# Optimization experiments

Hardware: AMD Instinct MI355X
Metric: run time of the kernel (lower is better)

## Reference

```python
import jax, jax.numpy as jnp
import numpy as np

B, N, F, E = 2048, 64, 32, 5
U1, U2, UA = 128, 64, 128

def setup_inputs() -> dict:
    key = jax.random.key(0)
    ks = jax.random.split(key, 16)
    inp = {
        'adjacency': jax.random.uniform(ks[0], (B, N, N, E), dtype=jnp.float32),
        'hidden': jnp.zeros((B, 1), dtype=jnp.float32),
        'node': jax.random.normal(ks[1], (B, N, F), dtype=jnp.float32),
        # conv layer 1: per-edge-type dense F->U1 (stacked), plus node dense F->U1
        'W1': jax.random.normal(ks[2], (E - 1, F, U1), dtype=jnp.float32) * 0.05,
        'b1': jnp.zeros((E - 1, U1), dtype=jnp.float32),
        'V1': jax.random.normal(ks[3], (F, U1), dtype=jnp.float32) * 0.05,
        'c1': jnp.zeros((U1,), dtype=jnp.float32),
        # conv layer 2: annotations (U1+F)->U2, node F->U2
        'W2': jax.random.normal(ks[4], (E - 1, U1 + F, U2), dtype=jnp.float32) * 0.05,
        'b2': jnp.zeros((E - 1, U2), dtype=jnp.float32),
        'V2': jax.random.normal(ks[5], (F, U2), dtype=jnp.float32) * 0.05,
        'c2': jnp.zeros((U2,), dtype=jnp.float32),
        # aggregation: (U2+F)->UA gates
        'Wi': jax.random.normal(ks[6], (U2 + F, UA), dtype=jnp.float32) * 0.05,
        'bi': jnp.zeros((UA,), dtype=jnp.float32),
        'Wj': jax.random.normal(ks[7], (U2 + F, UA), dtype=jnp.float32) * 0.05,
        'bj': jnp.zeros((UA,), dtype=jnp.float32),
    }
    return inp


def _gconv(adj_t, annotations, node, W, b, V, c):
    # adj_t: [B,E-1,N,N]; annotations: [B,N,Fa]; node: [B,N,F]
    h = jnp.einsum('bnf,efu->benu', annotations, W) + b[None, :, None, :]
    h = jnp.einsum('bemn,benu->bemu', adj_t, h)          # adjacency-weighted sum
    out = h.sum(axis=1) + node @ V + c                   # [B,N,U]
    return jnp.tanh(out)


def reference(adjacency, hidden, node, W1, b1, V1, c1, W2, b2, V2, c2, Wi, bi, Wj, bj):
    # drop edge type 0, transpose to [B,E-1,N,N]
    adj_t = jnp.transpose(adjacency[:, :, :, 1:], (0, 3, 1, 2))
    # hidden is rank-2 at entry -> first layer uses node only
    h1 = _gconv(adj_t, node, node, W1, b1, V1, c1)                       # [B,N,U1]
    h2 = _gconv(adj_t, jnp.concatenate((h1, node), -1), node, W2, b2, V2, c2)  # [B,N,U2]
    # encoder-level annotations: (output, node) since hidden is rank-2
    ann = jnp.concatenate((h2, node), -1)                                # [B,N,U2+F]
    i = jax.nn.sigmoid(ann @ Wi + bi)
    j = jnp.tanh(ann @ Wj + bj)
    out = jnp.tanh(jnp.sum(i * j, axis=1))                               # [B,UA]
    return out
```

## Files before the change

kernel.cpp:

```cpp
#include <hip/hip_runtime.h>

typedef _Float16 f16;
typedef f16  f16x8 __attribute__((ext_vector_type(8)));
typedef f16  f16x4 __attribute__((ext_vector_type(4)));
typedef float f32x4 __attribute__((ext_vector_type(4)));
typedef unsigned int u32;

#define W1T_HI 0
#define W1T_LO 16384
#define V1T_HI 32768
#define V1T_LO 36864
#define W2T_HI 40960
#define W2T_LO 81920
#define V2T_HI 122880
#define V2T_LO 124928
#define WIT_HI 126976
#define WIT_LO 139264
#define WJT_HI 151552
#define WJT_LO 163840
#define WS_SRC 88064

#define ADJB_HI 0
#define ADJB_LO 32768
#define ANNB_HI 49152
#define ANNB_LO 65536
#define PTB     73728
#define LDS_BYTES 81920

__device__ __forceinline__ f32x4 mfma16(f16x8 a, f16x8 b, f32x4 c){
  return __builtin_amdgcn_mfma_f32_16x16x32_f16(a, b, c, 0, 0, 0);
}
__device__ __forceinline__ float fast_tanh(float x){
  float e = __expf(2.f * x);
  return 1.f - 2.f * __builtin_amdgcn_rcpf(e + 1.f);
}
__device__ __forceinline__ float fast_sigmoid(float x){
  return __builtin_amdgcn_rcpf(1.f + __expf(-x));
}

__device__ __forceinline__ unsigned char enc1(float lo){
  f16 h = (f16)lo;
  unsigned short u = __builtin_bit_cast(unsigned short, h);
  return (unsigned char)(((u32)u + 0x80u) >> 8);
}
__device__ __forceinline__ void enc8(unsigned char* p, const float* lo){
  u32 a = 0, b = 0;
  #pragma unroll
  for (int j = 0; j < 4; ++j) a |= (u32)enc1(lo[j]) << (8*j);
  #pragma unroll
  for (int j = 0; j < 4; ++j) b |= (u32)enc1(lo[4+j]) << (8*j);
  uint2 v = {a, b};
  *(uint2*)p = v;
}
__device__ __forceinline__ u32 enc4(const float* lo){
  return (u32)enc1(lo[0]) | ((u32)enc1(lo[1]) << 8)
       | ((u32)enc1(lo[2]) << 16) | ((u32)enc1(lo[3]) << 24);
}
__device__ __forceinline__ f16x8 dec8(const unsigned char* p){
  uint2 d = *(const uint2*)p;
  u32 w[4];
  w[0] = __builtin_amdgcn_perm(0u, d.x, 0x010c000cu);
  w[1] = __builtin_amdgcn_perm(0u, d.x, 0x030c020cu);
  w[2] = __builtin_amdgcn_perm(0u, d.y, 0x010c000cu);
  w[3] = __builtin_amdgcn_perm(0u, d.y, 0x030c020cu);
  f16x8 r; __builtin_memcpy(&r, w, 16);
  return r;
}

__global__ void prep_weights(const float* __restrict__ W1, const float* __restrict__ V1,
                             const float* __restrict__ W2, const float* __restrict__ V2,
                             const float* __restrict__ Wi, const float* __restrict__ Wj,
                             f16* __restrict__ ws){
  int i = blockIdx.x * 256 + threadIdx.x;
  if (i >= WS_SRC) return;
  float v; int hi_off, lo_off, idx;
  int j = i;
  if (j < 16384){ int e = j >> 12, u = (j >> 5) & 127, f = j & 31;
    v = W1[(e*32 + f)*128 + u]; hi_off = W1T_HI; lo_off = W1T_LO; idx = j; }
  else if ((j -= 16384) < 4096){ int u = j >> 5, f = j & 31;
    v = V1[f*128 + u]; hi_off = V1T_HI; lo_off = V1T_LO; idx = j; }
  else if ((j -= 4096) < 40960){ int e = j / 10240, r = j % 10240, u = r / 160, k = r % 160;
    v = W2[e*10240 + k*64 + u]; hi_off = W2T_HI; lo_off = W2T_LO; idx = j; }
  else if ((j -= 40960) < 2048){ int u = j >> 5, f = j & 31;
    v = V2[f*64 + u]; hi_off = V2T_HI; lo_off = V2T_LO; idx = j; }
  else if ((j -= 2048) < 12288){ int ua = j / 96, k = j % 96;
    v = Wi[k*128 + ua]; hi_off = WIT_HI; lo_off = WIT_LO; idx = j; }
  else { j -= 12288; int ua = j / 96, k = j % 96;
    v = Wj[k*128 + ua]; hi_off = WJT_HI; lo_off = WJT_LO; idx = j; }
  f16 h = (f16)v;
  ws[hi_off + idx] = h;
  ws[lo_off + idx] = (f16)(v - (float)h);
}

__global__ __launch_bounds__(256, 2) void encoder_main(
    const float* __restrict__ adj, const float* __restrict__ node,
    const float* __restrict__ b1, const float* __restrict__ c1,
    const float* __restrict__ b2, const float* __restrict__ c2,
    const float* __restrict__ bi, const float* __restrict__ bj,
    const f16* __restrict__ wb, float* __restrict__ out)
{
  extern __shared__ unsigned char ldsb[];
  f16* adjh            = (f16*)(ldsb + ADJB_HI);
  unsigned char* adjl  = ldsb + ADJB_LO;
  f16* annh            = (f16*)(ldsb + ANNB_HI);
  unsigned char* annl  = ldsb + ANNB_LO;
  unsigned char* ptb   = ldsb + PTB;
  f16* nodeH           = (f16*)(ldsb + PTB);
  f16* nodeLo          = (f16*)(ldsb + PTB + 4096);

  const int tid  = threadIdx.x;
  const int w    = tid >> 6;
  const int lane = tid & 63;
  const int q    = lane >> 4;
  const int l15  = lane & 15;
  const int b    = blockIdx.x;
  const f32x4 z4 = {0.f, 0.f, 0.f, 0.f};

  {
    const float* ap = adj + (size_t)b * 20480;
    #pragma unroll
    for (int i = 0; i < 8; ++i){
      int fu = tid + 256*i;
      int e = fu >> 9, m = (fu >> 3) & 63, uc = fu & 7;
      const float* p = ap + (m*64 + uc*8)*5 + e + 1;
      float v[8], lo[8]; f16x8 hi;
      #pragma unroll
      for (int jj = 0; jj < 8; ++jj) v[jj] = p[jj*5];
      #pragma unroll
      for (int jj = 0; jj < 8; ++jj){
        f16 h = (f16)v[jj]; hi[jj] = h; lo[jj] = v[jj] - (float)h;
      }
      int off = e*4096 + m*64 + ((uc ^ (m & 7)) * 8);
      *(f16x8*)&adjh[off] = hi;
      enc8(&adjl[off], lo);
    }
    const float* np = node + (size_t)b * 2048 + (tid & 63)*32 + (tid >> 6)*8;
    float4 a = *(const float4*)np, c = *(const float4*)(np + 4);
    float v[8] = {a.x, a.y, a.z, a.w, c.x, c.y, c.z, c.w};
    f16x8 hi, lo;
    #pragma unroll
    for (int jj = 0; jj < 8; ++jj){
      f16 h = (f16)v[jj]; hi[jj] = h; lo[jj] = (f16)(v[jj] - (float)h);
    }
    int n = tid & 63, un = tid >> 6;
    *(f16x8*)&nodeH [n*32 + ((un ^ (n & 3)) * 8)] = hi;
    *(f16x8*)&nodeLo[n*32 + ((un ^ (n & 3)) * 8)] = lo;
  }
  __syncthreads();

  f16x8 anh[4], anl[4];
  #pragma unroll
  for (int mt = 0; mt < 4; ++mt){
    anh[mt] = *(const f16x8*)&nodeH [(mt*16 + l15)*32 + ((q ^ (l15 & 3)) * 8)];
    anl[mt] = *(const f16x8*)&nodeLo[(mt*16 + l15)*32 + ((q ^ (l15 & 3)) * 8)];
  }
  __syncthreads();

  const int ptrow  = (w*16 + l15) * 128;
  const int ptlrow = (w*16 + l15) * 128;

  f32x4 acc1[4][2];
  #pragma unroll
  for (int mt = 0; mt < 4; ++mt){ acc1[mt][0] = z4; acc1[mt][1] = z4; }

  #pragma unroll
  for (int e = 0; e < 4; ++e){
    f16x8 ah[2][4], al[2][4];
    #pragma unroll
    for (int ks = 0; ks < 2; ++ks)
      #pragma unroll
      for (int mt = 0; mt < 4; ++mt){
        int off = e*4096 + (mt*16 + l15)*64 + (((ks*4 + q) ^ (l15 & 7)) * 8);
        ah[ks][mt] = *(const f16x8*)&adjh[off];
        al[ks][mt] = dec8(&adjl[off]);
      }
    #pragma unroll
    for (int ut = 0; ut < 2; ++ut){
      const int u = w*32 + ut*16 + l15;
      f16x8 wh = *(const f16x8*)&wb[W1T_HI + (e*128 + u)*32 + q*8];
      f16x8 wl = *(const f16x8*)&wb[W1T_LO + (e*128 + u)*32 + q*8];
      float bias = b1[e*128 + u];
      #pragma unroll
      for (int mt = 0; mt < 4; ++mt){
        f32x4 pf = mfma16(anh[mt], wh, z4);
        pf = mfma16(anl[mt], wh, pf);
        pf = mfma16(anh[mt], wl, pf);
        f16x4 ph; float lo4[4];
        #pragma unroll
        for (int r = 0; r < 4; ++r){
          float v = pf[r] + bias;
          f16 h = (f16)v; ph[r] = h; lo4[r] = v - (float)h;
        }
        int unit = ((mt*2 + (q >> 1)) ^ (l15 & 7));
        *(f16x4*)(ptb + ptrow + unit*16 + (q & 1)*8) = ph;
        *(u32*)(annl + ptlrow + unit*8 + (q & 1)*4) = enc4(lo4);
      }
      #pragma unroll
      for (int ks = 0; ks < 2; ++ks){
        int pu = ((ks*4 + q) ^ (l15 & 7));
        f16x8 bph = *(const f16x8*)(ptb + ptrow + pu*16);
        f16x8 bpl = dec8(annl + ptlrow + pu*8);
        #pragma unroll
        for (int mt = 0; mt < 4; ++mt){
          acc1[mt][ut] = mfma16(ah[ks][mt], bph, acc1[mt][ut]);
          acc1[mt][ut] = mfma16(al[ks][mt], bph, acc1[mt][ut]);
          acc1[mt][ut] = mfma16(ah[ks][mt], bpl, acc1[mt][ut]);
        }
      }
    }
  }
  __syncthreads();

  #pragma unroll
  for (int ut = 0; ut < 2; ++ut){
    const int u = w*32 + ut*16 + l15;
    f16x8 wh = *(const f16x8*)&wb[V1T_HI + u*32 + q*8];
    f16x8 wl = *(const f16x8*)&wb[V1T_LO + u*32 + q*8];
    float cv = c1[u];
    #pragma unroll
    for (int mt = 0; mt < 4; ++mt){
      f32x4 a = acc1[mt][ut];
      a = mfma16(anh[mt], wh, a);
      a = mfma16(anl[mt], wh, a);
      a = mfma16(anh[mt], wl, a);
      #pragma unroll
      for (int r = 0; r < 4; ++r){
        float h = fast_tanh(a[r] + cv);
        f16 hh = (f16)h;
        int row = mt*16 + q*4 + r;
        int unit = ((u >> 3) ^ (row & 7));
        annh[row*128 + unit*8 + (u & 7)] = hh;
        annl[row*128 + unit*8 + (u & 7)] = enc1(h - (float)hh);
      }
    }
  }
  __syncthreads();

  const int u2 = w*16 + l15;
  f32x4 qf[4][4];
  #pragma unroll
  for (int mt = 0; mt < 4; ++mt){
    f16x8 axh[4], axl[4];
    #pragma unroll
    for (int ks = 0; ks < 4; ++ks){
      int off = (mt*16 + l15)*128 + (((ks*4 + q) ^ (l15 & 7)) * 8);
      axh[ks] = *(const f16x8*)&annh[off];
      axl[ks] = dec8(&annl[off]);
    }
    #pragma unroll
    for (int e = 0; e < 4; ++e){
      const f16* w2h = &wb[W2T_HI + (e*64 + u2)*160];
      const f16* w2l = &wb[W2T_LO + (e*64 + u2)*160];
      f16x8 wnh = *(const f16x8*)&w2h[4*32 + q*8];
      f16x8 wnl = *(const f16x8*)&w2l[4*32 + q*8];
      f32x4 t = mfma16(anh[mt], wnh, z4);
      t = mfma16(anl[mt], wnh, t);
      t = mfma16(anh[mt], wnl, t);
      #pragma unroll
      for (int ks = 0; ks < 4; ++ks){
        f16x8 wh = *(const f16x8*)&w2h[ks*32 + q*8];
        f16x8 wl = *(const f16x8*)&w2l[ks*32 + q*8];
        t = mfma16(axh[ks], wh, t);
        t = mfma16(axl[ks], wh, t);
        t = mfma16(axh[ks], wl, t);
      }
      qf[e][mt] = t;
    }
  }
  __syncthreads();

  f32x4 acc2[4];
  #pragma unroll
  for (int mt = 0; mt < 4; ++mt) acc2[mt] = z4;
  #pragma unroll
  for (int e = 0; e < 4; ++e){
    float bias = b2[e*64 + u2];
    #pragma unroll
    for (int mt = 0; mt < 4; ++mt){
      f16x4 ph; float lo4[4];
      #pragma unroll
      for (int r = 0; r < 4; ++r){
        float v = qf[e][mt][r] + bias;
        f16 h = (f16)v; ph[r] = h; lo4[r] = v - (float)h;
      }
      int unit = ((mt*2 + (q >> 1)) ^ (l15 & 7));
      *(f16x4*)(ptb + ptrow + unit*16 + (q & 1)*8) = ph;
      *(u32*)(annl + ptlrow + unit*8 + (q & 1)*4) = enc4(lo4);
    }
    #pragma unroll
    for (int ks = 0; ks < 2; ++ks){
      int pu = ((ks*4 + q) ^ (l15 & 7));
      f16x8 bph = *(const f16x8*)(ptb + ptrow + pu*16);
      f16x8 bpl = dec8(annl + ptlrow + pu*8);
      #pragma unroll
      for (int mt = 0; mt < 4; ++mt){
        int off = e*4096 + (mt*16 + l15)*64 + (((ks*4 + q) ^ (l15 & 7)) * 8);
        f16x8 ah = *(const f16x8*)&adjh[off];
        f16x8 al = dec8(&adjl[off]);
        acc2[mt] = mfma16(ah, bph, acc2[mt]);
        acc2[mt] = mfma16(al, bph, acc2[mt]);
        acc2[mt] = mfma16(ah, bpl, acc2[mt]);
      }
    }
  }
  {
    f16x8 wh = *(const f16x8*)&wb[V2T_HI + u2*32 + q*8];
    f16x8 wl = *(const f16x8*)&wb[V2T_LO + u2*32 + q*8];
    #pragma unroll
    for (int mt = 0; mt < 4; ++mt){
      acc2[mt] = mfma16(anh[mt], wh, acc2[mt]);
      acc2[mt] = mfma16(anl[mt], wh, acc2[mt]);
      acc2[mt] = mfma16(anh[mt], wl, acc2[mt]);
    }
  }
  {
    float cv = c2[u2];
    const int uc = 64 + u2;
    #pragma unroll
    for (int mt = 0; mt < 4; ++mt)
      #pragma unroll
      for (int r = 0; r < 4; ++r){
        float h = fast_tanh(acc2[mt][r] + cv);
        f16 hh = (f16)h;
        int row = mt*16 + q*4 + r;
        int unit = ((uc >> 3) ^ (row & 7));
        annh[row*128 + unit*8 + (uc & 7)] = hh;
        annl[row*128 + unit*8 + (uc & 7)] = enc1(h - (float)hh);
      }
  }
  __syncthreads();

  f16x8 wih[2][3], wil[2][3], wjh[2][3], wjl[2][3];
  float bib[2], bjb[2];
  #pragma unroll
  for (int ut = 0; ut < 2; ++ut){
    const int ua = w*32 + ut*16 + l15;
    #pragma unroll
    for (int ks = 0; ks < 3; ++ks){
      wih[ut][ks] = *(const f16x8*)&wb[WIT_HI + ua*96 + ks*32 + q*8];
      wil[ut][ks] = *(const f16x8*)&wb[WIT_LO + ua*96 + ks*32 + q*8];
      wjh[ut][ks] = *(const f16x8*)&wb[WJT_HI + ua*96 + ks*32 + q*8];
      wjl[ut][ks] = *(const f16x8*)&wb[WJT_LO + ua*96 + ks*32 + q*8];
    }
    bib[ut] = bi[ua]; bjb[ut] = bj[ua];
  }
  float s[2] = {0.f, 0.f};
  #pragma unroll
  for (int mt = 0; mt < 4; ++mt){
    f16x8 gh[2], gl[2];
    #pragma unroll
    for (int ks = 0; ks < 2; ++ks){
      int off = (mt*16 + l15)*128 + (((8 + ks*4 + q) ^ (l15 & 7)) * 8);
      gh[ks] = *(const f16x8*)&annh[off];
      gl[ks] = dec8(&annl[off]);
    }
    #pragma unroll
    for (int ut = 0; ut < 2; ++ut){
      f32x4 ia = mfma16(anh[mt], wih[ut][2], z4);
      ia = mfma16(anl[mt], wih[ut][2], ia);
      ia = mfma16(anh[mt], wil[ut][2], ia);
      f32x4 ja = mfma16(anh[mt], wjh[ut][2], z4);
      ja = mfma16(anl[mt], wjh[ut][2], ja);
      ja = mfma16(anh[mt], wjl[ut][2], ja);
      #pragma unroll
      for (int ks = 0; ks < 2; ++ks){
        ia = mfma16(gh[ks], wih[ut][ks], ia);
        ia = mfma16(gl[ks], wih[ut][ks], ia);
        ia = mfma16(gh[ks], wil[ut][ks], ia);
        ja = mfma16(gh[ks], wjh[ut][ks], ja);
        ja = mfma16(gl[ks], wjh[ut][ks], ja);
        ja = mfma16(gh[ks], wjl[ut][ks], ja);
      }
      #pragma unroll
      for (int r = 0; r < 4; ++r)
        s[ut] += fast_sigmoid(ia[r] + bib[ut]) * fast_tanh(ja[r] + bjb[ut]);
    }
  }
  #pragma unroll
  for (int ut = 0; ut < 2; ++ut){
    float t = s[ut];
    t += __shfl_xor(t, 16);
    t += __shfl_xor(t, 32);
    if (q == 0) out[(size_t)b*128 + (w*32 + ut*16 + l15)] = fast_tanh(t);
  }
}

extern "C" void kernel_launch(void* const* d_in, const int* in_sizes, int n_in,
                              void* d_out, int out_size, void* d_ws, size_t ws_size,
                              hipStream_t stream) {
  (void)in_sizes; (void)n_in; (void)out_size; (void)ws_size;
  const float* adj  = (const float*)d_in[0];
  const float* node = (const float*)d_in[2];
  const float* W1   = (const float*)d_in[3];
  const float* b1   = (const float*)d_in[4];
  const float* V1   = (const float*)d_in[5];
  const float* c1   = (const float*)d_in[6];
  const float* W2   = (const float*)d_in[7];
  const float* b2   = (const float*)d_in[8];
  const float* V2   = (const float*)d_in[9];
  const float* c2   = (const float*)d_in[10];
  const float* Wi   = (const float*)d_in[11];
  const float* bi   = (const float*)d_in[12];
  const float* Wj   = (const float*)d_in[13];
  const float* bj   = (const float*)d_in[14];
  f16* wb    = (f16*)d_ws;
  float* out = (float*)d_out;

  hipFuncSetAttribute((const void*)encoder_main,
                      hipFuncAttributeMaxDynamicSharedMemorySize, LDS_BYTES);

  prep_weights<<<(WS_SRC + 255) / 256, 256, 0, stream>>>(W1, V1, W2, V2, Wi, Wj, wb);
  encoder_main<<<2048, 256, LDS_BYTES, stream>>>(adj, node, b1, c1, b2, c2, bi, bj, wb, out);
}
```

Before: 366.2 us.

## Split edge types across two wave groups with 512-thread blocks and LDS reduction

Doubles the block to 8 waves and splits the four edge types so each group of four waves handles two, then reduces the partial accumulators of both graph-conv layers through an LDS scratch buffer. Per-wave scratch for the intermediate products is remapped into the node and annotation regions, and the aggregation stage gives each wave 16 output units. The aim is more parallelism per sample to hide latency. The cost is extra barriers and LDS traffic for the cross-group reduction, plus higher register pressure under the new launch bounds.

```diff
diff --git a/kernel.cpp b/kernel.cpp
--- a/kernel.cpp
+++ b/kernel.cpp
@@ -92,7 +92,7 @@
   ws[lo_off + idx] = (f16)(v - (float)h);
 }
 
-__global__ __launch_bounds__(256, 2) void encoder_main(
+__global__ __launch_bounds__(512, 4) void encoder_main(
     const float* __restrict__ adj, const float* __restrict__ node,
     const float* __restrict__ b1, const float* __restrict__ c1,
     const float* __restrict__ b2, const float* __restrict__ c2,
@@ -104,7 +104,7 @@
   unsigned char* adjl  = ldsb + ADJB_LO;
   f16* annh            = (f16*)(ldsb + ANNB_HI);
   unsigned char* annl  = ldsb + ANNB_LO;
-  unsigned char* ptb   = ldsb + PTB;
+  float* scr           = (float*)(ldsb + ANNB_HI);
   f16* nodeH           = (f16*)(ldsb + PTB);
   f16* nodeLo          = (f16*)(ldsb + PTB + 4096);
 
@@ -113,14 +113,21 @@
   const int lane = tid & 63;
   const int q    = lane >> 4;
   const int l15  = lane & 15;
+  const int eg   = w >> 2;
+  const int w4   = w & 3;
   const int b    = blockIdx.x;
   const f32x4 z4 = {0.f, 0.f, 0.f, 0.f};
 
+  unsigned char* ptb = ldsb + ((w < 4) ? (PTB + w*2048) : (ANNB_HI + (w - 4)*2048));
+  unsigned char* ptl = ldsb + ANNB_LO + w*1024;
+  const int ptrow  = l15 * 128;
+  const int ptlrow = l15 * 64;
+
   {
     const float* ap = adj + (size_t)b * 20480;
     #pragma unroll
-    for (int i = 0; i < 8; ++i){
-      int fu = tid + 256*i;
+    for (int i = 0; i < 4; ++i){
+      int fu = tid + 512*i;
       int e = fu >> 9, m = (fu >> 3) & 63, uc = fu & 7;
       const float* p = ap + (m*64 + uc*8)*5 + e + 1;
       float v[8], lo[8]; f16x8 hi;
@@ -134,17 +141,19 @@
       *(f16x8*)&adjh[off] = hi;
       enc8(&adjl[off], lo);
     }
-    const float* np = node + (size_t)b * 2048 + (tid & 63)*32 + (tid >> 6)*8;
-    float4 a = *(const float4*)np, c = *(const float4*)(np + 4);
-    float v[8] = {a.x, a.y, a.z, a.w, c.x, c.y, c.z, c.w};
-    f16x8 hi, lo;
-    #pragma unroll
-    for (int jj = 0; jj < 8; ++jj){
-      f16 h = (f16)v[jj]; hi[jj] = h; lo[jj] = (f16)(v[jj] - (float)h);
-    }
-    int n = tid & 63, un = tid >> 6;
-    *(f16x8*)&nodeH [n*32 + ((un ^ (n & 3)) * 8)] = hi;
-    *(f16x8*)&nodeLo[n*32 + ((un ^ (n & 3)) * 8)] = lo;
+    if (tid < 256){
+      const float* np = node + (size_t)b * 2048 + (tid & 63)*32 + (tid >> 6)*8;
+      float4 a = *(const float4*)np, c = *(const float4*)(np + 4);
+      float v[8] = {a.x, a.y, a.z, a.w, c.x, c.y, c.z, c.w};
+      f16x8 hi, lo;
+      #pragma unroll
+      for (int jj = 0; jj < 8; ++jj){
+        f16 h = (f16)v[jj]; hi[jj] = h; lo[jj] = (f16)(v[jj] - (float)h);
+      }
+      int n = tid & 63, un = tid >> 6;
+      *(f16x8*)&nodeH [n*32 + ((un ^ (n & 3)) * 8)] = hi;
+      *(f16x8*)&nodeLo[n*32 + ((un ^ (n & 3)) * 8)] = lo;
+    }
   }
   __syncthreads();
 
@@ -156,15 +165,13 @@
   }
   __syncthreads();
 
-  const int ptrow  = (w*16 + l15) * 128;
-  const int ptlrow = (w*16 + l15) * 128;
-
   f32x4 acc1[4][2];
   #pragma unroll
   for (int mt = 0; mt < 4; ++mt){ acc1[mt][0] = z4; acc1[mt][1] = z4; }
 
   #pragma unroll
-  for (int e = 0; e < 4; ++e){
+  for (int i = 0; i < 2; ++i){
+    const int e = eg*2 + i;
     f16x8 ah[2][4], al[2][4];
     #pragma unroll
     for (int ks = 0; ks < 2; ++ks)
@@ -176,7 +183,7 @@
       }
     #pragma unroll
     for (int ut = 0; ut < 2; ++ut){
-      const int u = w*32 + ut*16 + l15;
+      const int u = w4*32 + ut*16 + l15;
       f16x8 wh = *(const f16x8*)&wb[W1T_HI + (e*128 + u)*32 + q*8];
       f16x8 wl = *(const f16x8*)&wb[W1T_LO + (e*128 + u)*32 + q*8];
       float bias = b1[e*128 + u];
@@ -193,13 +200,13 @@
         }
         int unit = ((mt*2 + (q >> 1)) ^ (l15 & 7));
         *(f16x4*)(ptb + ptrow + unit*16 + (q & 1)*8) = ph;
-        *(u32*)(annl + ptlrow + unit*8 + (q & 1)*4) = enc4(lo4);
+        *(u32*)(ptl + ptlrow + unit*8 + (q & 1)*4) = enc4(lo4);
       }
       #pragma unroll
       for (int ks = 0; ks < 2; ++ks){
         int pu = ((ks*4 + q) ^ (l15 & 7));
         f16x8 bph = *(const f16x8*)(ptb + ptrow + pu*16);
-        f16x8 bpl = dec8(annl + ptlrow + pu*8);
+        f16x8 bpl = dec8(ptl + ptlrow + pu*8);
         #pragma unroll
         for (int mt = 0; mt < 4; ++mt){
           acc1[mt][ut] = mfma16(ah[ks][mt], bph, acc1[mt][ut]);
@@ -211,33 +218,67 @@
   }
   __syncthreads();
 
-  #pragma unroll
-  for (int ut = 0; ut < 2; ++ut){
-    const int u = w*32 + ut*16 + l15;
-    f16x8 wh = *(const f16x8*)&wb[V1T_HI + u*32 + q*8];
-    f16x8 wl = *(const f16x8*)&wb[V1T_LO + u*32 + q*8];
-    float cv = c1[u];
-    #pragma unroll
-    for (int mt = 0; mt < 4; ++mt){
-      f32x4 a = acc1[mt][ut];
-      a = mfma16(anh[mt], wh, a);
-      a = mfma16(anl[mt], wh, a);
-      a = mfma16(anh[mt], wl, a);
-      #pragma unroll
-      for (int r = 0; r < 4; ++r){
-        float h = fast_tanh(a[r] + cv);
-        f16 hh = (f16)h;
-        int row = mt*16 + q*4 + r;
-        int unit = ((u >> 3) ^ (row & 7));
-        annh[row*128 + unit*8 + (u & 7)] = hh;
-        annl[row*128 + unit*8 + (u & 7)] = enc1(h - (float)hh);
-      }
-    }
-  }
-  __syncthreads();
-
-  const int u2 = w*16 + l15;
-  f32x4 qf[4][4];
+  if (eg == 0){
+    #pragma unroll
+    for (int ut = 0; ut < 2; ++ut){
+      const int u = w4*32 + ut*16 + l15;
+      f16x8 wh = *(const f16x8*)&wb[V1T_HI + u*32 + q*8];
+      f16x8 wl = *(const f16x8*)&wb[V1T_LO + u*32 + q*8];
+      #pragma unroll
+      for (int mt = 0; mt < 4; ++mt){
+        acc1[mt][ut] = mfma16(anh[mt], wh, acc1[mt][ut]);
+        acc1[mt][ut] = mfma16(anl[mt], wh, acc1[mt][ut]);
+        acc1[mt][ut] = mfma16(anh[mt], wl, acc1[mt][ut]);
+      }
+    }
+  } else {
+    #pragma unroll
+    for (int mt = 0; mt < 4; ++mt)
+      #pragma unroll
+      for (int ut = 0; ut < 2; ++ut)
+        #pragma unroll
+        for (int r = 0; r < 4; ++r){
+          int n = mt*16 + q*4 + r;
+          int u = w4*32 + ut*16 + l15;
+          scr[n*128 + (u ^ ((n & 4) << 2))] = acc1[mt][ut][r];
+        }
+  }
+  __syncthreads();
+  if (eg == 0){
+    #pragma unroll
+    for (int mt = 0; mt < 4; ++mt)
+      #pragma unroll
+      for (int ut = 0; ut < 2; ++ut)
+        #pragma unroll
+        for (int r = 0; r < 4; ++r){
+          int n = mt*16 + q*4 + r;
+          int u = w4*32 + ut*16 + l15;
+          acc1[mt][ut][r] += scr[n*128 + (u ^ ((n & 4) << 2))];
+        }
+  }
+  __syncthreads();
+  if (eg == 0){
+    #pragma unroll
+    for (int ut = 0; ut < 2; ++ut){
+      const int u = w4*32 + ut*16 + l15;
+      float cv = c1[u];
+      #pragma unroll
+      for (int mt = 0; mt < 4; ++mt)
+        #pragma unroll
+        for (int r = 0; r < 4; ++r){
+          float h = fast_tanh(acc1[mt][ut][r] + cv);
+          f16 hh = (f16)h;
+          int row = mt*16 + q*4 + r;
+          int unit = ((u >> 3) ^ (row & 7));
+          annh[row*128 + unit*8 + (u & 7)] = hh;
+          annl[row*128 + unit*8 + (u & 7)] = enc1(h - (float)hh);
+        }
+    }
+  }
+  __syncthreads();
+
+  const int u2 = w4*16 + l15;
+  f32x4 qf[2][4];
   #pragma unroll
   for (int mt = 0; mt < 4; ++mt){
     f16x8 axh[4], axl[4];
@@ -248,7 +289,8 @@
       axl[ks] = dec8(&annl[off]);
     }
     #pragma unroll
-    for (int e = 0; e < 4; ++e){
+    for (int i = 0; i < 2; ++i){
+      const int e = eg*2 + i;
       const f16* w2h = &wb[W2T_HI + (e*64 + u2)*160];
       const f16* w2l = &wb[W2T_LO + (e*64 + u2)*160];
       f16x8 wnh = *(const f16x8*)&w2h[4*32 + q*8];
@@ -264,7 +306,7 @@
         t = mfma16(axl[ks], wh, t);
         t = mfma16(axh[ks], wl, t);
       }
-      qf[e][mt] = t;
+      qf[i][mt] = t;
     }
   }
   __syncthreads();
@@ -273,25 +315,26 @@
   #pragma unroll
   for (int mt = 0; mt < 4; ++mt) acc2[mt] = z4;
   #pragma unroll
-  for (int e = 0; e < 4; ++e){
+  for (int i = 0; i < 2; ++i){
+    const int e = eg*2 + i;
     float bias = b2[e*64 + u2];
     #pragma unroll
     for (int mt = 0; mt < 4; ++mt){
       f16x4 ph; float lo4[4];
       #pragma unroll
       for (int r = 0; r < 4; ++r){
-        float v = qf[e][mt][r] + bias;
+        float v = qf[i][mt][r] + bias;
         f16 h = (f16)v; ph[r] = h; lo4[r] = v - (float)h;
       }
       int unit = ((mt*2 + (q >> 1)) ^ (l15 & 7));
       *(f16x4*)(ptb + ptrow + unit*16 + (q & 1)*8) = ph;
-      *(u32*)(annl + ptlrow + unit*8 + (q & 1)*4) = enc4(lo4);
+      *(u32*)(ptl + ptlrow + unit*8 + (q & 1)*4) = enc4(lo4);
     }
     #pragma unroll
     for (int ks = 0; ks < 2; ++ks){
       int pu = ((ks*4 + q) ^ (l15 & 7));
       f16x8 bph = *(const f16x8*)(ptb + ptrow + pu*16);
-      f16x8 bpl = dec8(annl + ptlrow + pu*8);
+      f16x8 bpl = dec8(ptl + ptlrow + pu*8);
       #pragma unroll
       for (int mt = 0; mt < 4; ++mt){
         int off = e*4096 + (mt*16 + l15)*64 + (((ks*4 + q) ^ (l15 & 7)) * 8);
@@ -303,7 +346,8 @@
       }
     }
   }
-  {
+  __syncthreads();
+  if (eg == 0){
     f16x8 wh = *(const f16x8*)&wb[V2T_HI + u2*32 + q*8];
     f16x8 wl = *(const f16x8*)&wb[V2T_LO + u2*32 + q*8];
     #pragma unroll
@@ -312,8 +356,27 @@
       acc2[mt] = mfma16(anl[mt], wh, acc2[mt]);
       acc2[mt] = mfma16(anh[mt], wl, acc2[mt]);
     }
-  }
-  {
+  } else {
+    #pragma unroll
+    for (int mt = 0; mt < 4; ++mt)
+      #pragma unroll
+      for (int r = 0; r < 4; ++r){
+        int n = mt*16 + q*4 + r;
+        scr[n*64 + (u2 ^ ((n & 4) << 2))] = acc2[mt][r];
+      }
+  }
+  __syncthreads();
+  if (eg == 0){
+    #pragma unroll
+    for (int mt = 0; mt < 4; ++mt)
+      #pragma unroll
+      for (int r = 0; r < 4; ++r){
+        int n = mt*16 + q*4 + r;
+        acc2[mt][r] += scr[n*64 + (u2 ^ ((n & 4) << 2))];
+      }
+  }
+  __syncthreads();
+  if (eg == 0){
     float cv = c2[u2];
     const int uc = 64 + u2;
     #pragma unroll
@@ -330,21 +393,17 @@
   }
   __syncthreads();
 
-  f16x8 wih[2][3], wil[2][3], wjh[2][3], wjl[2][3];
-  float bib[2], bjb[2];
-  #pragma unroll
-  for (int ut = 0; ut < 2; ++ut){
-    const int ua = w*32 + ut*16 + l15;
-    #pragma unroll
-    for (int ks = 0; ks < 3; ++ks){
-      wih[ut][ks] = *(const f16x8*)&wb[WIT_HI + ua*96 + ks*32 + q*8];
-      wil[ut][ks] = *(const f16x8*)&wb[WIT_LO + ua*96 + ks*32 + q*8];
-      wjh[ut][ks] = *(const f16x8*)&wb[WJT_HI + ua*96 + ks*32 + q*8];
-      wjl[ut][ks] = *(const f16x8*)&wb[WJT_LO + ua*96 + ks*32 + q*8];
-    }
-    bib[ut] = bi[ua]; bjb[ut] = bj[ua];
-  }
-  float s[2] = {0.f, 0.f};
+  const int ua = w*16 + l15;
+  f16x8 wih[3], wil[3], wjh[3], wjl[3];
+  #pragma unroll
+  for (int ks = 0; ks < 3; ++ks){
+    wih[ks] = *(const f16x8*)&wb[WIT_HI + ua*96 + ks*32 + q*8];
+    wil[ks] = *(const f16x8*)&wb[WIT_LO + ua*96 + ks*32 + q*8];
+    wjh[ks] = *(const f16x8*)&wb[WJT_HI + ua*96 + ks*32 + q*8];
+    wjl[ks] = *(const f16x8*)&wb[WJT_LO + ua*96 + ks*32 + q*8];
+  }
+  float bib = bi[ua], bjb = bj[ua];
+  float s = 0.f;
   #pragma unroll
   for (int mt = 0; mt < 4; ++mt){
     f16x8 gh[2], gl[2];
@@ -354,35 +413,28 @@
       gh[ks] = *(const f16x8*)&annh[off];
       gl[ks] = dec8(&annl[off]);
     }
-    #pragma unroll
-    for (int ut = 0; ut < 2; ++ut){
-      f32x4 ia = mfma16(anh[mt], wih[ut][2], z4);
-      ia = mfma16(anl[mt], wih[ut][2], ia);
-      ia = mfma16(anh[mt], wil[ut][2], ia);
-      f32x4 ja = mfma16(anh[mt], wjh[ut][2], z4);
-      ja = mfma16(anl[mt], wjh[ut][2], ja);
-      ja = mfma16(anh[mt], wjl[ut][2], ja);
-      #pragma unroll
-      for (int ks = 0; ks < 2; ++ks){
-        ia = mfma16(gh[ks], wih[ut][ks], ia);
-        ia = mfma16(gl[ks], wih[ut][ks], ia);
-        ia = mfma16(gh[ks], wil[ut][ks], ia);
-        ja = mfma16(gh[ks], wjh[ut][ks], ja);
-        ja = mfma16(gl[ks], wjh[ut][ks], ja);
-        ja = mfma16(gh[ks], wjl[ut][ks], ja);
-      }
-      #pragma unroll
-      for (int r = 0; r < 4; ++r)
-        s[ut] += fast_sigmoid(ia[r] + bib[ut]) * fast_tanh(ja[r] + bjb[ut]);
-    }
-  }
-  #pragma unroll
-  for (int ut = 0; ut < 2; ++ut){
-    float t = s[ut];
-    t += __shfl_xor(t, 16);
-    t += __shfl_xor(t, 32);
-    if (q == 0) out[(size_t)b*128 + (w*32 + ut*16 + l15)] = fast_tanh(t);
-  }
+    f32x4 ia = mfma16(anh[mt], wih[2], z4);
+    ia = mfma16(anl[mt], wih[2], ia);
+    ia = mfma16(anh[mt], wil[2], ia);
+    f32x4 ja = mfma16(anh[mt], wjh[2], z4);
+    ja = mfma16(anl[mt], wjh[2], ja);
+    ja = mfma16(anh[mt], wjl[2], ja);
+    #pragma unroll
+    for (int ks = 0; ks < 2; ++ks){
+      ia = mfma16(gh[ks], wih[ks], ia);
+      ia = mfma16(gl[ks], wih[ks], ia);
+      ia = mfma16(gh[ks], wil[ks], ia);
+      ja = mfma16(gh[ks], wjh[ks], ja);
+      ja = mfma16(gl[ks], wjh[ks], ja);
+      ja = mfma16(gh[ks], wjl[ks], ja);
+    }
+    #pragma unroll
+    for (int r = 0; r < 4; ++r)
+      s += fast_sigmoid(ia[r] + bib) * fast_tanh(ja[r] + bjb);
+  }
+  s += __shfl_xor(s, 16);
+  s += __shfl_xor(s, 32);
+  if (q == 0) out[(size_t)b*128 + ua] = fast_tanh(s);
 }
 
 extern "C" void kernel_launch(void* const* d_in, const int* in_sizes, int n_in,
@@ -410,5 +462,5 @@
                       hipFuncAttributeMaxDynamicSharedMemorySize, LDS_BYTES);
 
   prep_weights<<<(WS_SRC + 255) / 256, 256, 0, stream>>>(W1, V1, W2, V2, Wi, Wj, wb);
-  encoder_main<<<2048, 256, LDS_BYTES, stream>>>(adj, node, b1, c1, b2, c2, bi, bj, wb, out);
-}
+  encoder_main<<<2048, 512, LDS_BYTES, stream>>>(adj, node, b1, c1, b2, c2, bi, bj, wb, out);
+}
```

Result: slower. 502.8 us (+37.3%).
